# Kernel optimization log

Measured on AMD Instinct MI355X. Metric: run time of the kernel, lower is better.

Reference implementation:

```python
import jax, jax.numpy as jnp
import numpy as np

NUM_EMBEDDINGS = 8192
EMBEDDING_DIM = 256
COMMITMENT_COST = 0.25


def setup_inputs() -> dict:
    key = jax.random.key(0)
    k1, k2 = jax.random.split(key)
    z_e = jax.random.normal(k1, (32, EMBEDDING_DIM, 32, 32), dtype=jnp.float32)
    # nn.init.uniform_(weight, -1/K, 1/K)
    bound = 1.0 / NUM_EMBEDDINGS
    emb_w = jax.random.uniform(k2, (NUM_EMBEDDINGS, EMBEDDING_DIM), dtype=jnp.float32,
                               minval=-bound, maxval=bound)
    return {"z_e": z_e, "emb_w": emb_w}


def reference(z_e, emb_w):
    b, c, h, w = z_e.shape
    orig_dtype = z_e.dtype
    z = z_e.astype(jnp.float32)
    emb = emb_w.astype(jnp.float32)
    # [B,C,H,W] -> [N, C]
    z_flat = z.transpose(0, 2, 3, 1).reshape(-1, c)
    distances = (jnp.sum(z_flat * z_flat, axis=1, keepdims=True)
                 - 2.0 * (z_flat @ emb.T)
                 + jnp.sum(emb * emb, axis=1))
    encoding_indices = jnp.argmin(distances, axis=1)  # [N]
    z_q = emb[encoding_indices].reshape(b, h, w, c).transpose(0, 3, 1, 2)
    # eval path: commitment = cc * mse(stop_grad(z_e), z_q); codebook = mse(...)
    mse = jnp.mean((jax.lax.stop_gradient(z) - z_q) ** 2)
    vq_loss = (1.0 + COMMITMENT_COST) * mse
    # straight-through estimator
    z_q_st = (z + jax.lax.stop_gradient(z_q - z)).astype(orig_dtype)
    # perplexity from code usage histogram
    n_tokens = encoding_indices.shape[0]
    counts = jnp.zeros((NUM_EMBEDDINGS,), jnp.float32).at[encoding_indices].add(1.0)
    avg_probs = counts / n_tokens
    perplexity = jnp.exp(-jnp.sum(avg_probs * jnp.log(jnp.clip(avg_probs, 1e-10, None))))
    indices = encoding_indices.reshape(b, h, w)
    return z_q_st, vq_loss, perplexity, indices
```

## Files before the change

kernel.cpp:

```cpp
#include <hip/hip_runtime.h>
#include <hip/hip_fp16.h>
#include <cmath>
#include <float.h>

#define NUM_EMB 8192
#define DIM 256
#define HW 1024
#define N_TOK 32768
#define KSPLIT 2
#define KRANGE (NUM_EMB/KSPLIT)
#define OUT_ZQ_ELEMS 8388608

#define CAP 24
#define MARGIN_GP 0.4f

#define BM 128
#define BN 128
#define TILES (KRANGE/BN)

#define WS_MSE    0
#define WS_COUNTS 64
#define WS_CNT    (WS_COUNTS + NUM_EMB*4)
#define WS_MEMSET_END (WS_CNT + KSPLIT*N_TOK*4)
#define WS_Z2     WS_MEMSET_END
#define WS_CANDI  (WS_Z2 + N_TOK*4)

typedef _Float16 half8 __attribute__((ext_vector_type(8)));
typedef _Float16 half4v __attribute__((ext_vector_type(4)));
typedef float f32x16 __attribute__((ext_vector_type(16)));
typedef __attribute__((address_space(3))) void lds_void;
typedef __attribute__((address_space(1))) const void gbl_void;

__global__ __launch_bounds__(256) void vq_pack_z(
    const float* __restrict__ z, _Float16* __restrict__ zh, float* __restrict__ z2)
{
    __shared__ float zt[32][257];
    __shared__ float rr[32][16];
    int t = threadIdx.x;
    int n0 = blockIdx.x * 32;
    int b = n0 >> 10, hw0 = n0 & 1023;
    const float* zb = z + (size_t)b * DIM * HW + hw0;
    int tn = t & 31, tc = t >> 5;
    #pragma unroll 4
    for (int it = 0; it < 32; it++) {
        int c = it * 8 + tc;
        zt[tn][c] = zb[(size_t)c * HW + tn];
    }
    __syncthreads();
    int tn2 = t & 31, tj = t >> 5;
    #pragma unroll
    for (int h = 0; h < 2; h++) {
        float v0 = zt[tn2][h*128 + tj];
        float r = __fmul_rn(v0, v0);
        for (int i = 8; i < 128; i += 8) {
            float v = zt[tn2][h*128 + i + tj];
            r = __fadd_rn(r, __fmul_rn(v, v));
        }
        rr[tn2][h*8 + tj] = r;
    }
    int row = t >> 3, seg = t & 7;
    half8 outv[4];
    #pragma unroll
    for (int q = 0; q < 4; q++)
        #pragma unroll
        for (int u = 0; u < 8; u++)
            outv[q][u] = (_Float16)zt[row][seg*32 + q*8 + u];
    half8* dst = (half8*)(zh + (size_t)(n0 + row) * DIM + seg * 32);
    #pragma unroll
    for (int q = 0; q < 4; q++) dst[q] = outv[q];
    __syncthreads();
    if (t < 32) {
        const float* rw = rr[t];
        float h0 = __fadd_rn(__fadd_rn(__fadd_rn(rw[0], rw[1]), __fadd_rn(rw[2], rw[3])),
                             __fadd_rn(__fadd_rn(rw[4], rw[5]), __fadd_rn(rw[6], rw[7])));
        float h1 = __fadd_rn(__fadd_rn(__fadd_rn(rw[8], rw[9]), __fadd_rn(rw[10], rw[11])),
                             __fadd_rn(__fadd_rn(rw[12], rw[13]), __fadd_rn(rw[14], rw[15])));
        z2[n0 + t] = __fadd_rn(h0, h1);
    }
}

__global__ __launch_bounds__(256) void vq_pack_e(
    const float* __restrict__ emb, _Float16* __restrict__ eh)
{
    int i = blockIdx.x * 256 + threadIdx.x;
    float4 v = ((const float4*)emb)[i];
    half4v h;
    h[0] = (_Float16)(v.x * 8192.0f);
    h[1] = (_Float16)(v.y * 8192.0f);
    h[2] = (_Float16)(v.z * 8192.0f);
    h[3] = (_Float16)(v.w * 8192.0f);
    *(half4v*)(eh + (size_t)i * 4) = h;
}

__global__ __launch_bounds__(256, 2) void vq_dist_kernel(
    const _Float16* __restrict__ zh, const _Float16* __restrict__ eh,
    int* __restrict__ cnt, int* __restrict__ candi)
{
    __shared__ _Float16 Bs[2][16384];
    int t = threadIdx.x;
    int w = t >> 6, lane = t & 63;
    int lm = lane & 31, lh = lane >> 5;
    int n0 = blockIdx.x * BM;
    int ks = blockIdx.y;
    int kbase = ks * KRANGE;

    const _Float16* arow = zh + (size_t)(n0 + w*32 + lm) * DIM + lh * 8;
    half8 Areg[16];
    #pragma unroll
    for (int s = 0; s < 16; s++)
        Areg[s] = *(const half8*)(arow + s * 16);

    int scode[8], soct[8];
    #pragma unroll
    for (int r = 0; r < 8; r++) {
        int p = r * 256 + t;
        scode[r] = p >> 5;
        soct[r]  = ((p & 31) - (p >> 5)) & 31;
    }

    #pragma unroll
    for (int r = 0; r < 8; r++)
        __builtin_amdgcn_global_load_lds(
            (gbl_void*)(eh + (size_t)(kbase + scode[r]) * DIM + soct[r] * 8),
            (lds_void*)((char*)&Bs[0][0] + (r*256 + t) * 16), 16, 0, 0);

    float rmax[4][4];
    #pragma unroll
    for (int g = 0; g < 4; g++)
        #pragma unroll
        for (int ro = 0; ro < 4; ro++) rmax[g][ro] = -1e30f;

    int cl0 = lm, cl1 = 32 + lm;
    for (int tile = 0; tile < TILES; tile++) {
        f32x16 acc0, acc1, acc2, acc3;
        #pragma unroll
        for (int e = 0; e < 16; e++) { acc0[e]=0.f; acc1[e]=0.f; acc2[e]=0.f; acc3[e]=0.f; }

        #pragma unroll
        for (int h = 0; h < 2; h++) {
            __syncthreads();
            int Sn = tile*2 + h + 1;
            if (Sn < 2*TILES) {
                int cb = kbase + (Sn >> 1) * BN + (Sn & 1) * 64;
                #pragma unroll
                for (int r = 0; r < 8; r++)
                    __builtin_amdgcn_global_load_lds(
                        (gbl_void*)(eh + (size_t)(cb + scode[r]) * DIM + soct[r] * 8),
                        (lds_void*)((char*)&Bs[h^1][0] + (r*256 + t) * 16), 16, 0, 0);
            }
            #pragma unroll
            for (int s = 0; s < 16; s++) {
                int o = s*2 + lh;
                half8 b0 = *(const half8*)(&Bs[h][0] + ((cl0*32 + ((o + cl0) & 31)) * 8));
                half8 b1 = *(const half8*)(&Bs[h][0] + ((cl1*32 + ((o + cl1) & 31)) * 8));
                if (h == 0) {
                    acc0 = __builtin_amdgcn_mfma_f32_32x32x16_f16(Areg[s], b0, acc0, 0, 0, 0);
                    acc1 = __builtin_amdgcn_mfma_f32_32x32x16_f16(Areg[s], b1, acc1, 0, 0, 0);
                } else {
                    acc2 = __builtin_amdgcn_mfma_f32_32x32x16_f16(Areg[s], b0, acc2, 0, 0, 0);
                    acc3 = __builtin_amdgcn_mfma_f32_32x32x16_f16(Areg[s], b1, acc3, 0, 0, 0);
                }
            }
        }

        int cb = kbase + tile * BN;
        #pragma unroll
        for (int g = 0; g < 4; g++) {
            #pragma unroll
            for (int ro = 0; ro < 4; ro++) {
                int e = g*4 + ro;
                float vm = fmaxf(fmaxf(acc0[e], acc1[e]), fmaxf(acc2[e], acc3[e]));
                float rm = vm;
                rm = fmaxf(rm, __shfl_xor(rm, 1));
                rm = fmaxf(rm, __shfl_xor(rm, 2));
                rm = fmaxf(rm, __shfl_xor(rm, 4));
                rm = fmaxf(rm, __shfl_xor(rm, 8));
                rm = fmaxf(rm, __shfl_xor(rm, 16));
                rmax[g][ro] = fmaxf(rmax[g][ro], rm);
                float cut = rmax[g][ro] - MARGIN_GP;
                if (fmaxf(fmaxf(acc0[e], acc1[e]), fmaxf(acc2[e], acc3[e])) > cut) {
                    int token = n0 + w*32 + 4*lh + 8*g + ro;
                    int idx   = ks * N_TOK + token;
                    if (acc0[e] > cut) {
                        int slot = atomicAdd(&cnt[idx], 1);
                        if (slot < CAP) candi[(size_t)idx * CAP + slot] = cb + lm;
                    }
                    if (acc1[e] > cut) {
                        int slot = atomicAdd(&cnt[idx], 1);
                        if (slot < CAP) candi[(size_t)idx * CAP + slot] = cb + 32 + lm;
                    }
                    if (acc2[e] > cut) {
                        int slot = atomicAdd(&cnt[idx], 1);
                        if (slot < CAP) candi[(size_t)idx * CAP + slot] = cb + 64 + lm;
                    }
                    if (acc3[e] > cut) {
                        int slot = atomicAdd(&cnt[idx], 1);
                        if (slot < CAP) candi[(size_t)idx * CAP + slot] = cb + 96 + lm;
                    }
                }
            }
        }
    }
}

#define GT 32
__global__ __launch_bounds__(256) void vq_rg_kernel(
    const float* __restrict__ z, const float* __restrict__ emb,
    const float* __restrict__ z2, const int* __restrict__ cnt,
    const int* __restrict__ candi,
    int* __restrict__ counts, double* __restrict__ mse_sum,
    float* __restrict__ out_zq, float* __restrict__ out_idx)
{
    __shared__ float zs[GT][257];
    __shared__ float zq[GT][DIM];
    __shared__ unsigned long long kmin[GT];
    __shared__ int sidx[GT];
    __shared__ double red[4];
    int t = threadIdx.x;
    int n0 = blockIdx.x * GT;
    int b = n0 >> 10, hw0 = n0 & 1023;
    int lane = t & 63, w = t >> 6;

    {
        int nn = t & 31, cg = t >> 5;
        const float* zb = z + (size_t)b * DIM * HW + hw0 + nn;
        #pragma unroll 4
        for (int i = 0; i < 32; i++) {
            int c = i*8 + cg;
            zs[nn][c] = zb[(size_t)c * HW];
        }
    }
    if (t < GT) kmin[t] = ~0ULL;
    __syncthreads();

    int tcs0[8], po[9];
    int ovf8 = 0;
    po[0] = 0;
    #pragma unroll
    for (int i = 0; i < 8; i++) {
        int n = n0 + w*8 + i;
        int c0 = cnt[n], c1 = cnt[N_TOK + n];
        if (c0 > CAP || c1 > CAP) { c0 = 0; c1 = 0; ovf8 |= (1 << i); }
        tcs0[i] = c0;
        po[i+1] = po[i] + c0 + c1;
    }
    int total = po[8];

    for (int base = 0; base < total; base += 64) {
        int g = base + lane;
        unsigned long long key = ~0ULL;
        int mytok = -1;
        if (g < total) {
            int i = 0;
            #pragma unroll
            for (int q = 1; q < 8; q++) i += (g >= po[q]);
            int sl = g - po[i];
            int n = n0 + w*8 + i;
            int s = sl >= tcs0[i];
            int slot = s ? sl - tcs0[i] : sl;
            int code = candi[((size_t)s * N_TOK + n) * CAP + slot];
            int tok = w*8 + i;
            float accv = 0.f;
            const float4* ep = (const float4*)(emb + (size_t)code * DIM);
            #pragma unroll 8
            for (int q4 = 0; q4 < 64; q4++) {
                float4 e4 = ep[q4];
                accv = fmaf(zs[tok][q4*4+0], e4.x, accv);
                accv = fmaf(zs[tok][q4*4+1], e4.y, accv);
                accv = fmaf(zs[tok][q4*4+2], e4.z, accv);
                accv = fmaf(zs[tok][q4*4+3], e4.w, accv);
            }
            float d = fmaf(-2.f, accv, z2[n]);
            key = ((unsigned long long)__float_as_uint(d) << 32) | (unsigned)code;
            mytok = tok;
        }
        #pragma unroll
        for (int i = 0; i < 8; i++) {
            unsigned long long kk = (mytok == w*8 + i) ? key : ~0ULL;
            #pragma unroll
            for (int o = 32; o > 0; o >>= 1) {
                unsigned long long ob = __shfl_xor(kk, o);
                if (ob < kk) kk = ob;
            }
            if (lane == 0 && kk < kmin[w*8 + i]) kmin[w*8 + i] = kk;
        }
    }

    for (int i = 0; i < 8; i++) if (ovf8 & (1 << i)) {
        int tok = w*8 + i, n = n0 + tok;
        float z2n = z2[n];
        unsigned long long bst = ~0ULL;
        for (int k = lane; k < NUM_EMB; k += 64) {
            float accv = 0.f;
            const float4* ep = (const float4*)(emb + (size_t)k * DIM);
            #pragma unroll 8
            for (int q4 = 0; q4 < 64; q4++) {
                float4 e4 = ep[q4];
                accv = fmaf(zs[tok][q4*4+0], e4.x, accv);
                accv = fmaf(zs[tok][q4*4+1], e4.y, accv);
                accv = fmaf(zs[tok][q4*4+2], e4.z, accv);
                accv = fmaf(zs[tok][q4*4+3], e4.w, accv);
            }
            float d = fmaf(-2.f, accv, z2n);
            unsigned long long kk =
                ((unsigned long long)__float_as_uint(d) << 32) | (unsigned)k;
            if (kk < bst) bst = kk;
        }
        #pragma unroll
        for (int o = 32; o > 0; o >>= 1) {
            unsigned long long ob = __shfl_xor(bst, o);
            if (ob < bst) bst = ob;
        }
        if (lane == 0 && bst < kmin[tok]) kmin[tok] = bst;
    }
    __syncthreads();

    if (t < GT) {
        int bi = (int)(kmin[t] & 0xffffffffu);
        sidx[t] = bi;
        out_idx[n0 + t] = (float)bi;
        atomicAdd(&counts[bi], 1);
    }
    __syncthreads();

    for (int m = w*8; m < w*8 + 8; m++) {
        int row = sidx[m];
        float4 v = *(const float4*)(emb + (size_t)row * DIM + lane * 4);
        int cb = (lane + m) & 63;
        *(float4*)&zq[m][cb * 4] = v;
    }
    __syncthreads();

    int nn = t & 31, cc = t >> 5;
    float* op = out_zq + (size_t)b * DIM * HW + hw0 + nn;
    float lsum = 0.f;
    #pragma unroll 4
    for (int i = 0; i < 32; i++) {
        int c = i*8 + cc;
        int cb = ((c >> 2) + nn) & 63;
        float q = zq[nn][cb*4 + (c & 3)];
        float zv = zs[nn][c];
        op[(size_t)c * HW] = __fadd_rn(zv, __fsub_rn(q, zv));
        float d = zv - q;
        lsum = fmaf(d, d, lsum);
    }
    double ds = (double)lsum;
    #pragma unroll
    for (int off = 32; off > 0; off >>= 1)
        ds += __shfl_down(ds, off);
    if (lane == 0) red[w] = ds;
    __syncthreads();
    if (t == 0) atomicAdd(mse_sum, red[0] + red[1] + red[2] + red[3]);
}

__global__ __launch_bounds__(256) void vq_finalize_kernel(
    const double* __restrict__ mse_sum, const int* __restrict__ counts,
    float* __restrict__ out_scalars)
{
    __shared__ float red[4];
    int t = threadIdx.x;
    float local = 0.f;
    for (int k = t; k < NUM_EMB; k += 256) {
        int c = counts[k];
        if (c > 0) {
            float p = (float)c * (1.0f / (float)N_TOK);
            local += p * logf(p);
        }
    }
    int lane = t & 63, w = t >> 6;
    #pragma unroll
    for (int off = 32; off > 0; off >>= 1)
        local += __shfl_down(local, off);
    if (lane == 0) red[w] = local;
    __syncthreads();
    if (t == 0) {
        float s = red[0] + red[1] + red[2] + red[3];
        out_scalars[0] = 1.25f * (float)(*mse_sum * (1.0 / (double)OUT_ZQ_ELEMS));
        out_scalars[1] = expf(-s);
    }
}

extern "C" void kernel_launch(void* const* d_in, const int* in_sizes, int n_in,
                              void* d_out, int out_size, void* d_ws, size_t ws_size,
                              hipStream_t stream)
{
    const float* z   = (const float*)d_in[0];
    const float* emb = (const float*)d_in[1];
    float* out = (float*)d_out;
    char* ws = (char*)d_ws;
    double* mse_sum = (double*)(ws + WS_MSE);
    int*    counts  = (int*)(ws + WS_COUNTS);
    int*    cnt     = (int*)(ws + WS_CNT);
    float*  z2      = (float*)(ws + WS_Z2);
    int*    candi   = (int*)(ws + WS_CANDI);

    _Float16* zh = (_Float16*)d_out;
    _Float16* eh = (_Float16*)(out + 4194304);

    hipMemsetAsync(d_ws, 0, WS_MEMSET_END, stream);

    vq_pack_e<<<NUM_EMB*DIM/4/256, 256, 0, stream>>>(emb, eh);
    vq_pack_z<<<N_TOK/32, 256, 0, stream>>>(z, zh, z2);
    vq_dist_kernel<<<dim3(N_TOK/BM, KSPLIT), 256, 0, stream>>>(zh, eh, cnt, candi);
    vq_rg_kernel<<<N_TOK/GT, 256, 0, stream>>>(z, emb, z2, cnt, candi,
                                               counts, mse_sum,
                                               out, out + OUT_ZQ_ELEMS + 2);
    vq_finalize_kernel<<<1, 256, 0, stream>>>(mse_sum, counts, out + OUT_ZQ_ELEMS);
}
```

Before: 453.4 us.

## Split codebook four ways and halve LDS tiles to raise occupancy

Raises the codebook split from two to four, so twice as many blocks cover the distance GEMM. Each block now stages 32-code chunks in a smaller double-buffered LDS array and issues one MFMA per step instead of two. Launch bounds move to three blocks per CU. The refine kernel now merges candidates from four partitions, which means more candidate lists and extra count reads. The running max is kept per partition, so more codes may pass the margin test, adding atomics and raising overflow risk.

```diff
diff --git a/kernel.cpp b/kernel.cpp
--- a/kernel.cpp
+++ b/kernel.cpp
@@ -7,7 +7,7 @@
 #define DIM 256
 #define HW 1024
 #define N_TOK 32768
-#define KSPLIT 2
+#define KSPLIT 4
 #define KRANGE (NUM_EMB/KSPLIT)
 #define OUT_ZQ_ELEMS 8388608
 
@@ -16,7 +16,9 @@
 
 #define BM 128
 #define BN 128
+#define HC 32
 #define TILES (KRANGE/BN)
+#define NSTEP (KRANGE/HC)
 
 #define WS_MSE    0
 #define WS_COUNTS 64
@@ -92,11 +94,11 @@
     *(half4v*)(eh + (size_t)i * 4) = h;
 }
 
-__global__ __launch_bounds__(256, 2) void vq_dist_kernel(
+__global__ __launch_bounds__(256, 3) void vq_dist_kernel(
     const _Float16* __restrict__ zh, const _Float16* __restrict__ eh,
     int* __restrict__ cnt, int* __restrict__ candi)
 {
-    __shared__ _Float16 Bs[2][16384];
+    __shared__ _Float16 Bs[2][8192];
     int t = threadIdx.x;
     int w = t >> 6, lane = t & 63;
     int lm = lane & 31, lh = lane >> 5;
@@ -110,16 +112,16 @@
     for (int s = 0; s < 16; s++)
         Areg[s] = *(const half8*)(arow + s * 16);
 
-    int scode[8], soct[8];
-    #pragma unroll
-    for (int r = 0; r < 8; r++) {
+    int scode[4], soct[4];
+    #pragma unroll
+    for (int r = 0; r < 4; r++) {
         int p = r * 256 + t;
         scode[r] = p >> 5;
         soct[r]  = ((p & 31) - (p >> 5)) & 31;
     }
 
     #pragma unroll
-    for (int r = 0; r < 8; r++)
+    for (int r = 0; r < 4; r++)
         __builtin_amdgcn_global_load_lds(
             (gbl_void*)(eh + (size_t)(kbase + scode[r]) * DIM + soct[r] * 8),
             (lds_void*)((char*)&Bs[0][0] + (r*256 + t) * 16), 16, 0, 0);
@@ -130,36 +132,31 @@
         #pragma unroll
         for (int ro = 0; ro < 4; ro++) rmax[g][ro] = -1e30f;
 
-    int cl0 = lm, cl1 = 32 + lm;
     for (int tile = 0; tile < TILES; tile++) {
         f32x16 acc0, acc1, acc2, acc3;
         #pragma unroll
         for (int e = 0; e < 16; e++) { acc0[e]=0.f; acc1[e]=0.f; acc2[e]=0.f; acc3[e]=0.f; }
 
         #pragma unroll
-        for (int h = 0; h < 2; h++) {
+        for (int h = 0; h < 4; h++) {
             __syncthreads();
-            int Sn = tile*2 + h + 1;
-            if (Sn < 2*TILES) {
-                int cb = kbase + (Sn >> 1) * BN + (Sn & 1) * 64;
+            int Sn = tile*4 + h + 1;
+            if (Sn < NSTEP) {
+                int cb = kbase + Sn * HC;
                 #pragma unroll
-                for (int r = 0; r < 8; r++)
+                for (int r = 0; r < 4; r++)
                     __builtin_amdgcn_global_load_lds(
                         (gbl_void*)(eh + (size_t)(cb + scode[r]) * DIM + soct[r] * 8),
-                        (lds_void*)((char*)&Bs[h^1][0] + (r*256 + t) * 16), 16, 0, 0);
+                        (lds_void*)((char*)&Bs[(h&1)^1][0] + (r*256 + t) * 16), 16, 0, 0);
             }
             #pragma unroll
             for (int s = 0; s < 16; s++) {
                 int o = s*2 + lh;
-                half8 b0 = *(const half8*)(&Bs[h][0] + ((cl0*32 + ((o + cl0) & 31)) * 8));
-                half8 b1 = *(const half8*)(&Bs[h][0] + ((cl1*32 + ((o + cl1) & 31)) * 8));
-                if (h == 0) {
-                    acc0 = __builtin_amdgcn_mfma_f32_32x32x16_f16(Areg[s], b0, acc0, 0, 0, 0);
-                    acc1 = __builtin_amdgcn_mfma_f32_32x32x16_f16(Areg[s], b1, acc1, 0, 0, 0);
-                } else {
-                    acc2 = __builtin_amdgcn_mfma_f32_32x32x16_f16(Areg[s], b0, acc2, 0, 0, 0);
-                    acc3 = __builtin_amdgcn_mfma_f32_32x32x16_f16(Areg[s], b1, acc3, 0, 0, 0);
-                }
+                half8 b = *(const half8*)(&Bs[h&1][0] + ((lm*32 + ((o + lm) & 31)) * 8));
+                if (h == 0)      acc0 = __builtin_amdgcn_mfma_f32_32x32x16_f16(Areg[s], b, acc0, 0, 0, 0);
+                else if (h == 1) acc1 = __builtin_amdgcn_mfma_f32_32x32x16_f16(Areg[s], b, acc1, 0, 0, 0);
+                else if (h == 2) acc2 = __builtin_amdgcn_mfma_f32_32x32x16_f16(Areg[s], b, acc2, 0, 0, 0);
+                else             acc3 = __builtin_amdgcn_mfma_f32_32x32x16_f16(Areg[s], b, acc3, 0, 0, 0);
             }
         }
 
@@ -178,7 +175,7 @@
                 rm = fmaxf(rm, __shfl_xor(rm, 16));
                 rmax[g][ro] = fmaxf(rmax[g][ro], rm);
                 float cut = rmax[g][ro] - MARGIN_GP;
-                if (fmaxf(fmaxf(acc0[e], acc1[e]), fmaxf(acc2[e], acc3[e])) > cut) {
+                if (vm > cut) {
                     int token = n0 + w*32 + 4*lh + 8*g + ro;
                     int idx   = ks * N_TOK + token;
                     if (acc0[e] > cut) {
@@ -233,16 +230,21 @@
     if (t < GT) kmin[t] = ~0ULL;
     __syncthreads();
 
-    int tcs0[8], po[9];
+    int pc1[8], pc2[8], pc3[8], po[9];
     int ovf8 = 0;
     po[0] = 0;
     #pragma unroll
     for (int i = 0; i < 8; i++) {
         int n = n0 + w*8 + i;
-        int c0 = cnt[n], c1 = cnt[N_TOK + n];
-        if (c0 > CAP || c1 > CAP) { c0 = 0; c1 = 0; ovf8 |= (1 << i); }
-        tcs0[i] = c0;
-        po[i+1] = po[i] + c0 + c1;
+        int c0 = cnt[n];
+        int c1 = cnt[N_TOK + n];
+        int c2 = cnt[2*N_TOK + n];
+        int c3 = cnt[3*N_TOK + n];
+        if (c0 > CAP || c1 > CAP || c2 > CAP || c3 > CAP) {
+            c0 = c1 = c2 = c3 = 0; ovf8 |= (1 << i);
+        }
+        pc1[i] = c0; pc2[i] = c0 + c1; pc3[i] = c0 + c1 + c2;
+        po[i+1] = po[i] + c0 + c1 + c2 + c3;
     }
     int total = po[8];
 
@@ -256,8 +258,9 @@
             for (int q = 1; q < 8; q++) i += (g >= po[q]);
             int sl = g - po[i];
             int n = n0 + w*8 + i;
-            int s = sl >= tcs0[i];
-            int slot = s ? sl - tcs0[i] : sl;
+            int s = (sl >= pc1[i]) + (sl >= pc2[i]) + (sl >= pc3[i]);
+            int boff = (s == 0) ? 0 : ((s == 1) ? pc1[i] : ((s == 2) ? pc2[i] : pc3[i]));
+            int slot = sl - boff;
             int code = candi[((size_t)s * N_TOK + n) * CAP + slot];
             int tok = w*8 + i;
             float accv = 0.f;
```

Result: slower. 669.2 us (+47.6%).
